# Optimization experiments

Measured on AMD Instinct MI355X. Metric: run time of the kernel, lower is better.

The kernel has to match this reference:

```python
import jax, jax.numpy as jnp
import numpy as np

N = 100000      # patches per bag
L, H, D = 1024, 512, 256   # size_dict['small']
K = 64          # k_sample
NC = 2          # n_classes


def setup_inputs() -> dict:
    key = jax.random.key(0)
    ks = jax.random.split(key, 12)
    s = 0.02
    return {
        "h": jax.random.normal(ks[0], (N, L), dtype=jnp.float32),
        "W1": jax.random.normal(ks[1], (L, H), dtype=jnp.float32) * s,
        "b1": jnp.zeros((H,), jnp.float32),
        "Wa": jax.random.normal(ks[2], (H, D), dtype=jnp.float32) * s,
        "ba": jnp.zeros((D,), jnp.float32),
        "Wb": jax.random.normal(ks[3], (H, D), dtype=jnp.float32) * s,
        "bb": jnp.zeros((D,), jnp.float32),
        "Wc": jax.random.normal(ks[4], (D, 1), dtype=jnp.float32) * s,
        "bc": jnp.zeros((1,), jnp.float32),
        "Winst": jax.random.normal(ks[5], (H, 2), dtype=jnp.float32) * s,
        "binst": jnp.zeros((2,), jnp.float32),
        "Wcls": jax.random.normal(ks[6], (H, NC), dtype=jnp.float32) * s,
        "bcls": jnp.zeros((NC,), jnp.float32),
        "label": 1,
    }


def reference(h, W1, b1, Wa, ba, Wb, bb, Wc, bc, Winst, binst, Wcls, bcls, label):
    # fc: Linear(1024,512) + ReLU
    h1 = jax.nn.relu(h @ W1 + b1)                      # [N, 512]
    # gated attention net
    a = jnp.tanh(h1 @ Wa + ba)                         # [N, 256]
    g = jax.nn.sigmoid(h1 @ Wb + bb)                   # [N, 256]
    A = (a * g) @ Wc + bc                              # [N, 1]
    A = A.T                                            # [1, N]
    A_raw = A
    A = jax.nn.softmax(A, axis=1)                      # [1, N]

    # instance evaluation: top-k / bottom-k select + gather + tiny classifier
    Asq = A[0]                                         # [N]
    _, top_p_ids = jax.lax.top_k(Asq, K)
    _, top_n_ids = jax.lax.top_k(-Asq, K)
    all_inst = jnp.concatenate([h1[top_p_ids], h1[top_n_ids]], axis=0)  # [2K, 512]
    inst_logits = all_inst @ Winst + binst             # [2K, 2]
    all_preds = jnp.argmax(inst_logits, axis=1)
    p_targets = jnp.full((K,), label, dtype=jnp.int32)
    n_targets = jnp.zeros((K,), dtype=jnp.int32)
    all_targets = jnp.concatenate([p_targets, n_targets], axis=0)
    logp = jax.nn.log_softmax(inst_logits, axis=1)
    instance_loss = -jnp.mean(logp[jnp.arange(2 * K), all_targets])

    # bag-level aggregation and classifier
    M = A @ h1                                         # [1, 512]
    logits = M @ Wcls + bcls                           # [1, n_classes]
    Y_hat = jnp.argmax(logits, axis=1, keepdims=True)
    Y_prob = jax.nn.softmax(logits, axis=1)
    return logits, Y_prob, Y_hat, A_raw, instance_loss, all_preds, all_targets
```

## Files before the change

kernel.cpp:

```cpp
#include <hip/hip_runtime.h>

#define NN 100000
#define LL 1024
#define HH 512
#define DD 256
#define TOPK 64
#define CAP 3072
#define CPB 4

#define WS_W1T   0u
#define WS_B2    1048576u
#define WS_Z     1572864u
#define Z_MNUM   0u
#define Z_SEXP   2048u
#define Z_LOSS   2052u
#define Z_CNTT   2056u
#define Z_CNTB   2060u
#define Z_HIST   2064u
#define Z_WSA    10256u
#define Z_ZWORDS 102596
#define Z_PARAMS 410384u
#define Z_SEL    410392u
#define Z_CANDT  410944u
#define Z_CANDB  423232u
#define Z_AEXT   435520u
#define Z_AEXB   447808u

typedef float  f32x16 __attribute__((ext_vector_type(16)));
typedef short  bf16x8 __attribute__((ext_vector_type(8)));

#define MFMA(a,b,c) __builtin_amdgcn_mfma_f32_32x32x16_bf16(a,b,c,0,0,0)

__device__ __forceinline__ unsigned short f2bf(float x){
  unsigned u = __float_as_uint(x);
  u += 0x7FFFu + ((u >> 16) & 1u);
  return (unsigned short)(u >> 16);
}
__device__ __forceinline__ float bf2f(unsigned short v){
  return __uint_as_float(((unsigned)v) << 16);
}
__device__ __forceinline__ unsigned sortable_u(float f){
  unsigned u = __float_as_uint(f);
  return (u & 0x80000000u) ? ~u : (u | 0x80000000u);
}

__global__ void k0_prep(const float* __restrict__ W1, const float* __restrict__ Wa,
                        const float* __restrict__ Wb,
                        unsigned short* __restrict__ W1T, unsigned short* __restrict__ B2,
                        unsigned* __restrict__ zwords)
{
  const int n1 = HH * LL;
  const int n2 = HH * HH;
  const int tot = n1 + n2 + Z_ZWORDS;
  int stride = gridDim.x * 256;
  for (int idx = blockIdx.x * 256 + threadIdx.x; idx < tot; idx += stride){
    if (idx < n1){
      int n = idx >> 10, k = idx & 1023;
      W1T[idx] = f2bf(W1[k * HH + n]);
    } else if (idx < n1 + n2){
      int j = idx - n1;
      int n = j >> 9, k = j & 511;
      int w = n >> 6, ii = n & 63;
      float v = (ii < 32) ? Wa[k * DD + (w * 32 + ii)] : Wb[k * DD + (w * 32 + ii - 32)];
      B2[j] = f2bf(v);
    } else {
      zwords[idx - n1 - n2] = 0u;
    }
  }
}

__global__ __launch_bounds__(512, 2)
void k_mega(const float* __restrict__ h, const unsigned short* __restrict__ W1T,
            const unsigned short* __restrict__ B2g,
            const float* __restrict__ b1, const float* __restrict__ ba,
            const float* __restrict__ bbg, const float* __restrict__ Wc,
            const float* __restrict__ bc,
            float* __restrict__ outA,
            float* __restrict__ wsA,
            float* __restrict__ Mnum, float* __restrict__ sum_exp)
{
  __shared__ __align__(16) unsigned short SM[64 * 512];

  const int tid  = threadIdx.x;
  const int wid  = tid >> 6;
  const int lane = tid & 63;
  const int l31  = lane & 31;
  const int half = lane >> 5;
  const int r0   = blockIdx.x * 64;

  const int sr = tid >> 3;
  const int sc = (tid & 7) << 2;
  int gr = r0 + sr; if (gr > NN - 1) gr = NN - 1;
  const float* hp = h + (size_t)gr * LL + sc;

  const unsigned short* bp0 = W1T + (size_t)(wid * 64 + l31) * LL + half * 8;
  const unsigned short* bp1 = W1T + (size_t)(wid * 64 + 32 + l31) * LL + half * 8;

  f32x16 acc00 = (f32x16)0.f, acc01 = (f32x16)0.f, acc10 = (f32x16)0.f, acc11 = (f32x16)0.f;

  float4 av = *(const float4*)hp;
  #pragma unroll 1
  for (int kc = 0; kc < 32; ++kc){
    bf16x8 b00 = *(const bf16x8*)(bp0 + kc * 32);
    bf16x8 b01 = *(const bf16x8*)(bp0 + kc * 32 + 16);
    bf16x8 b10 = *(const bf16x8*)(bp1 + kc * 32);
    bf16x8 b11 = *(const bf16x8*)(bp1 + kc * 32 + 16);

    float4 cur = av;
    if (kc < 31) av = *(const float4*)(hp + (kc + 1) * 32);
    uint2 pk;
    pk.x = (unsigned)f2bf(cur.x) | ((unsigned)f2bf(cur.y) << 16);
    pk.y = (unsigned)f2bf(cur.z) | ((unsigned)f2bf(cur.w) << 16);
    __syncthreads();
    *(uint2*)(SM + sr * 40 + sc) = pk;
    __syncthreads();

    const unsigned short* a0p = SM + l31 * 40 + half * 8;
    const unsigned short* a1p = SM + (32 + l31) * 40 + half * 8;
    bf16x8 a0k0 = *(const bf16x8*)(a0p);
    bf16x8 a1k0 = *(const bf16x8*)(a1p);
    bf16x8 a0k1 = *(const bf16x8*)(a0p + 16);
    bf16x8 a1k1 = *(const bf16x8*)(a1p + 16);
    acc00 = MFMA(a0k0, b00, acc00); acc01 = MFMA(a0k0, b10, acc01);
    acc10 = MFMA(a1k0, b00, acc10); acc11 = MFMA(a1k0, b10, acc11);
    acc00 = MFMA(a0k1, b01, acc00); acc01 = MFMA(a0k1, b11, acc01);
    acc10 = MFMA(a1k1, b01, acc10); acc11 = MFMA(a1k1, b11, acc11);
  }
  __syncthreads();

  {
    float b1v0 = b1[wid * 64 + l31];
    float b1v1 = b1[wid * 64 + 32 + l31];
    int cb0 = wid * 8 + (l31 >> 3);
    int cb1 = wid * 8 + 4 + (l31 >> 3);
    int wi = l31 & 7;
    #pragma unroll
    for (int reg = 0; reg < 16; ++reg){
      int rA = (reg & 3) + ((reg >> 2) << 3) + (half << 2);
      int rB = rA + 32;
      float v;
      v = fmaxf(acc00[reg] + b1v0, 0.f); SM[rA * 512 + ((cb0 ^ (rA & 7)) << 3) + wi] = f2bf(v);
      v = fmaxf(acc01[reg] + b1v1, 0.f); SM[rA * 512 + ((cb1 ^ (rA & 7)) << 3) + wi] = f2bf(v);
      v = fmaxf(acc10[reg] + b1v0, 0.f); SM[rB * 512 + ((cb0 ^ (rB & 7)) << 3) + wi] = f2bf(v);
      v = fmaxf(acc11[reg] + b1v1, 0.f); SM[rB * 512 + ((cb1 ^ (rB & 7)) << 3) + wi] = f2bf(v);
    }
  }
  __syncthreads();

  f32x16 q00 = (f32x16)0.f, q01 = (f32x16)0.f, q10 = (f32x16)0.f, q11 = (f32x16)0.f;
  const unsigned short* c0p = B2g + (size_t)(wid * 64 + l31) * HH + half * 8;
  const unsigned short* c1p = B2g + (size_t)(wid * 64 + 32 + l31) * HH + half * 8;
  const int m0x = l31 & 7;
  #pragma unroll 1
  for (int kc = 0; kc < 16; ++kc){
    #pragma unroll
    for (int ks = 0; ks < 2; ++ks){
      int ko = kc * 32 + ks * 16;
      int sw = (((kc * 4 + ks * 2 + half) ^ m0x) << 3);
      bf16x8 a0 = *(const bf16x8*)(SM + l31 * 512 + sw);
      bf16x8 a1 = *(const bf16x8*)(SM + (32 + l31) * 512 + sw);
      bf16x8 b0 = *(const bf16x8*)(c0p + ko);
      bf16x8 b1 = *(const bf16x8*)(c1p + ko);
      q00 = MFMA(a0, b0, q00); q01 = MFMA(a0, b1, q01);
      q10 = MFMA(a1, b0, q10); q11 = MFMA(a1, b1, q11);
    }
  }

  {
    int ca = wid * 32 + l31;
    float bav = ba[ca], bbv = bbg[ca], wcv = Wc[ca];
    #pragma unroll
    for (int mt = 0; mt < 2; ++mt){
      #pragma unroll
      for (int reg = 0; reg < 16; ++reg){
        float pav = (mt ? q10[reg] : q00[reg]) + bav;
        float pbv = (mt ? q11[reg] : q01[reg]) + bbv;
        float p = tanhf(pav) * (1.f / (1.f + expf(-pbv))) * wcv;
        p += __shfl_xor(p, 1, 64);  p += __shfl_xor(p, 2, 64);
        p += __shfl_xor(p, 4, 64);  p += __shfl_xor(p, 8, 64);
        p += __shfl_xor(p, 16, 64);
        if (l31 == 0){
          int rl = mt * 32 + (reg & 3) + ((reg >> 2) << 3) + (half << 2);
          atomicAdd(&wsA[r0 + rl], p);
        }
      }
    }
  }
  __syncthreads();
  if (tid < 64){
    int g = r0 + tid;
    if (g < NN){
      float Ar = atomicAdd(&wsA[g], 0.0f) + bc[0];
      outA[g] = Ar;
    }
  }
  __syncthreads();

  float ev = 0.f;
  { int g = r0 + lane; if (g < NN) ev = expf(outA[g]); }
  float pm = 0.f;
  const int tch = tid >> 3, twi = tid & 7;
  #pragma unroll 4
  for (int r = 0; r < 64; ++r){
    float e = __shfl(ev, r, 64);
    pm += e * bf2f(SM[r * 512 + ((tch ^ (r & 7)) << 3) + twi]);
  }
  atomicAdd(&Mnum[tid], pm);
  if (wid == 0){
    float s = ev;
    s += __shfl_xor(s, 1, 64);  s += __shfl_xor(s, 2, 64);  s += __shfl_xor(s, 4, 64);
    s += __shfl_xor(s, 8, 64);  s += __shfl_xor(s, 16, 64); s += __shfl_xor(s, 32, 64);
    if (lane == 0) atomicAdd(sum_exp, s);
  }
}

__global__ void k_hist(const float* __restrict__ A, unsigned* __restrict__ hist)
{
  __shared__ unsigned lh[2048];
  for (int i = threadIdx.x; i < 2048; i += 256) lh[i] = 0u;
  __syncthreads();
  for (int i = blockIdx.x * 256 + threadIdx.x; i < NN; i += gridDim.x * 256)
    atomicAdd(&lh[sortable_u(A[i]) >> 21], 1u);
  __syncthreads();
  for (int i = threadIdx.x; i < 2048; i += 256)
    if (lh[i]) atomicAdd(&hist[i], lh[i]);
}

__global__ void k_scan(const unsigned* __restrict__ hist, unsigned* __restrict__ params)
{
  if (threadIdx.x == 0){
    unsigned c = 0; int b = 2047;
    while (b >= 0){ c += hist[b]; if (c >= TOPK) break; --b; }
    if (b < 0) b = 0;
    int be = (b > 0) ? b - 1 : 0;
    params[0] = ((unsigned)be) << 21;
    c = 0; int b2 = 0;
    while (b2 < 2048){ c += hist[b2]; if (c >= TOPK) break; ++b2; }
    if (b2 > 2047) b2 = 2047;
    unsigned be2 = (unsigned)((b2 < 2047) ? b2 + 1 : 2047);
    params[1] = ((be2 + 1u) << 21) - 1u;
  }
}

__global__ void k_collect(const float* __restrict__ A, const unsigned* __restrict__ params,
                          unsigned* cntT, unsigned* cntB,
                          unsigned* __restrict__ candT, unsigned* __restrict__ candB)
{
  unsigned p0 = params[0], p1 = params[1];
  for (int i = blockIdx.x * 256 + threadIdx.x; i < NN; i += gridDim.x * 256){
    unsigned u = sortable_u(A[i]);
    if (u >= p0){ unsigned pos = atomicAdd(cntT, 1u); if (pos < CAP) candT[pos] = (unsigned)i; }
    if (u <= p1){ unsigned pos = atomicAdd(cntB, 1u); if (pos < CAP) candB[pos] = (unsigned)i; }
  }
}

__global__ __launch_bounds__(256)
void k_exact(const float* __restrict__ h, const float* __restrict__ W1, const float* __restrict__ b1,
             const float* __restrict__ Wa, const float* __restrict__ ba,
             const float* __restrict__ Wb, const float* __restrict__ bbg,
             const float* __restrict__ Wc, const float* __restrict__ bc,
             const unsigned* cntT, const unsigned* cntB,
             const unsigned* __restrict__ candT, const unsigned* __restrict__ candB,
             float* __restrict__ AexT, float* __restrict__ AexB)
{
  const int PB = CAP / CPB;
  int b = blockIdx.x;
  int side = (b >= PB) ? 1 : 0;
  int base = (side ? b - PB : b) * CPB;
  unsigned cnt = side ? *cntB : *cntT;
  if (cnt > CAP) cnt = CAP;
  if (base >= (int)cnt) return;
  int nc = min(CPB, (int)cnt - base);
  const unsigned* cand = side ? candB : candT;
  float* Aex = side ? AexB : AexT;

  __shared__ float hrow[CPB][LL];
  __shared__ float h1row[CPB][HH];
  __shared__ unsigned rows_s[CPB];
  __shared__ float red[4][CPB];
  int tid = threadIdx.x;
  if (tid < CPB) rows_s[tid] = cand[base + min(tid, nc - 1)];
  __syncthreads();
  for (int c = 0; c < CPB; ++c)
    ((float4*)hrow[c])[tid] = ((const float4*)(h + (size_t)rows_s[c] * LL))[tid];
  __syncthreads();

  float s0[CPB], s1[CPB];
  { float v0 = b1[tid], v1 = b1[tid + 256];
    #pragma unroll
    for (int c = 0; c < CPB; ++c){ s0[c] = v0; s1[c] = v1; } }
  for (int k = 0; k < LL; ++k){
    float w0 = W1[k * HH + tid];
    float w1 = W1[k * HH + tid + 256];
    #pragma unroll
    for (int c = 0; c < CPB; ++c){ float hv = hrow[c][k]; s0[c] += hv * w0; s1[c] += hv * w1; }
  }
  #pragma unroll
  for (int c = 0; c < CPB; ++c){
    h1row[c][tid] = fmaxf(s0[c], 0.f);
    h1row[c][tid + 256] = fmaxf(s1[c], 0.f);
  }
  __syncthreads();

  float pa[CPB], pb[CPB];
  float bav = ba[tid], bbv = bbg[tid], wcv = Wc[tid];
  #pragma unroll
  for (int c = 0; c < CPB; ++c){ pa[c] = bav; pb[c] = bbv; }
  for (int k = 0; k < HH; ++k){
    float wav = Wa[k * DD + tid];
    float wbv = Wb[k * DD + tid];
    #pragma unroll
    for (int c = 0; c < CPB; ++c){ float hv = h1row[c][k]; pa[c] += hv * wav; pb[c] += hv * wbv; }
  }
  int lane = tid & 63, w = tid >> 6;
  #pragma unroll
  for (int c = 0; c < CPB; ++c){
    float p = tanhf(pa[c]) * (1.f / (1.f + expf(-pb[c]))) * wcv;
    p += __shfl_xor(p, 1, 64);  p += __shfl_xor(p, 2, 64);  p += __shfl_xor(p, 4, 64);
    p += __shfl_xor(p, 8, 64);  p += __shfl_xor(p, 16, 64); p += __shfl_xor(p, 32, 64);
    if (lane == 0) red[w][c] = p;
  }
  __syncthreads();
  if (tid == 0)
    for (int c = 0; c < nc; ++c)
      Aex[base + c] = red[0][c] + red[1][c] + red[2][c] + red[3][c] + bc[0];
}

__global__ __launch_bounds__(256)
void k_select(const unsigned* cntT, const unsigned* cntB,
              const unsigned* __restrict__ candT, const unsigned* __restrict__ candB,
              const float* __restrict__ AexT, const float* __restrict__ AexB,
              unsigned* __restrict__ sel)
{
  __shared__ unsigned long long keys[CAP];
  __shared__ unsigned long long wmax[4];
  __shared__ unsigned long long best_s;
  int tid = threadIdx.x;
  for (int side = 0; side < 2; ++side){
    unsigned cnt = side ? *cntB : *cntT; if (cnt > CAP) cnt = CAP;
    const unsigned* cand = side ? candB : candT;
    const float* Aex = side ? AexB : AexT;
    for (int j = tid; j < (int)cnt; j += 256){
      unsigned su = sortable_u(Aex[j]);
      if (side) su = ~su;
      keys[j] = (((unsigned long long)su) << 32) | (unsigned long long)(0xFFFFFFFFu - cand[j]);
    }
    __syncthreads();
    for (int it = 0; it < TOPK; ++it){
      unsigned long long loc = 0ull;
      for (int j = tid; j < (int)cnt; j += 256){ unsigned long long k = keys[j]; loc = (k > loc) ? k : loc; }
      for (int off = 1; off < 64; off <<= 1){
        unsigned long long o = __shfl_xor(loc, off, 64);
        loc = (o > loc) ? o : loc;
      }
      if ((tid & 63) == 0) wmax[tid >> 6] = loc;
      __syncthreads();
      if (tid == 0){
        unsigned long long m01 = (wmax[0] > wmax[1]) ? wmax[0] : wmax[1];
        unsigned long long m23 = (wmax[2] > wmax[3]) ? wmax[2] : wmax[3];
        unsigned long long bb_ = (m01 > m23) ? m01 : m23;
        best_s = bb_;
        sel[side * TOPK + it] = 0xFFFFFFFFu - (unsigned)(bb_ & 0xFFFFFFFFull);
      }
      __syncthreads();
      unsigned long long bv = best_s;
      for (int j = tid; j < (int)cnt; j += 256) if (keys[j] == bv) keys[j] = 0ull;
      __syncthreads();
    }
    __syncthreads();
  }
}

__global__ __launch_bounds__(256)
void k_inst(const float* __restrict__ h, const float* __restrict__ W1, const float* __restrict__ b1,
            const float* __restrict__ Winst, const float* __restrict__ binst,
            const unsigned* __restrict__ sel, const int* __restrict__ labelp,
            float* __restrict__ out, float* __restrict__ loss_sum)
{
  __shared__ float hrow[LL];
  __shared__ float h1row[HH];
  __shared__ float red[4][2];
  int i = blockIdx.x, tid = threadIdx.x;
  unsigned row = sel[i];
  ((float4*)hrow)[tid] = ((const float4*)(h + (size_t)row * LL))[tid];
  __syncthreads();
  float s0 = b1[tid], s1 = b1[tid + 256];
  for (int k = 0; k < LL; ++k){
    float hv = hrow[k];
    s0 += hv * W1[k * HH + tid];
    s1 += hv * W1[k * HH + tid + 256];
  }
  h1row[tid] = fmaxf(s0, 0.f); h1row[tid + 256] = fmaxf(s1, 0.f);
  __syncthreads();
  float l0 = 0.f, l1 = 0.f;
  for (int d = tid; d < HH; d += 256){
    float hv = h1row[d];
    l0 += hv * Winst[d * 2];
    l1 += hv * Winst[d * 2 + 1];
  }
  for (int off = 1; off < 64; off <<= 1){ l0 += __shfl_xor(l0, off, 64); l1 += __shfl_xor(l1, off, 64); }
  if ((tid & 63) == 0){ red[tid >> 6][0] = l0; red[tid >> 6][1] = l1; }
  __syncthreads();
  if (tid == 0){
    float L0 = red[0][0] + red[1][0] + red[2][0] + red[3][0] + binst[0];
    float L1 = red[0][1] + red[1][1] + red[2][1] + red[3][1] + binst[1];
    int lab = labelp[0];
    int tgt = (i < TOPK) ? lab : 0;
    out[100006 + i] = (L1 > L0) ? 1.f : 0.f;
    out[100134 + i] = (float)tgt;
    float m = fmaxf(L0, L1);
    float lse = m + logf(expf(L0 - m) + expf(L1 - m));
    float lp = ((tgt == 1) ? L1 : L0) - lse;
    atomicAdd(loss_sum, -lp);
  }
}

__global__ __launch_bounds__(512)
void k_final(const float* __restrict__ Mnum, const float* __restrict__ sum_exp,
             const float* __restrict__ Wcls, const float* __restrict__ bcls,
             const float* __restrict__ loss_sum, float* __restrict__ out)
{
  __shared__ float red[8][2];
  int tid = threadIdx.x;
  float S = *sum_exp;
  float m = Mnum[tid] / S;
  float p0 = m * Wcls[tid * 2], p1 = m * Wcls[tid * 2 + 1];
  for (int off = 1; off < 64; off <<= 1){ p0 += __shfl_xor(p0, off, 64); p1 += __shfl_xor(p1, off, 64); }
  if ((tid & 63) == 0){ red[tid >> 6][0] = p0; red[tid >> 6][1] = p1; }
  __syncthreads();
  if (tid == 0){
    float L0 = bcls[0], L1 = bcls[1];
    for (int w = 0; w < 8; ++w){ L0 += red[w][0]; L1 += red[w][1]; }
    out[0] = L0; out[1] = L1;
    float mm = fmaxf(L0, L1);
    float e0 = expf(L0 - mm), e1 = expf(L1 - mm);
    out[2] = e0 / (e0 + e1); out[3] = e1 / (e0 + e1);
    out[4] = (L1 > L0) ? 1.f : 0.f;
    out[100005] = loss_sum[0] / 128.f;
  }
}

extern "C" void kernel_launch(void* const* d_in, const int* in_sizes, int n_in,
                              void* d_out, int out_size, void* d_ws, size_t ws_size,
                              hipStream_t stream)
{
  const float* h     = (const float*)d_in[0];
  const float* W1    = (const float*)d_in[1];
  const float* b1    = (const float*)d_in[2];
  const float* Wa    = (const float*)d_in[3];
  const float* ba    = (const float*)d_in[4];
  const float* Wb    = (const float*)d_in[5];
  const float* bbg   = (const float*)d_in[6];
  const float* Wc    = (const float*)d_in[7];
  const float* bc    = (const float*)d_in[8];
  const float* Winst = (const float*)d_in[9];
  const float* binst = (const float*)d_in[10];
  const float* Wcls  = (const float*)d_in[11];
  const float* bcls  = (const float*)d_in[12];
  const int*   label = (const int*)d_in[13];
  float* out = (float*)d_out;

  char* ws = (char*)d_ws;
  unsigned short* W1T = (unsigned short*)(ws + WS_W1T);
  unsigned short* B2  = (unsigned short*)(ws + WS_B2);
  char* Z = ws + WS_Z;
  float*    Mnum   = (float*)(Z + Z_MNUM);
  float*    sexp   = (float*)(Z + Z_SEXP);
  float*    lsum   = (float*)(Z + Z_LOSS);
  unsigned* cntT   = (unsigned*)(Z + Z_CNTT);
  unsigned* cntB   = (unsigned*)(Z + Z_CNTB);
  unsigned* hist   = (unsigned*)(Z + Z_HIST);
  float*    wsA    = (float*)(Z + Z_WSA);
  unsigned* params = (unsigned*)(Z + Z_PARAMS);
  unsigned* sel    = (unsigned*)(Z + Z_SEL);
  unsigned* candT  = (unsigned*)(Z + Z_CANDT);
  unsigned* candB  = (unsigned*)(Z + Z_CANDB);
  float*    AexT   = (float*)(Z + Z_AEXT);
  float*    AexB   = (float*)(Z + Z_AEXB);

  k0_prep<<<1024, 256, 0, stream>>>(W1, Wa, Wb, W1T, B2, (unsigned*)Z);
  k_mega<<<1563, 512, 0, stream>>>(h, W1T, B2, b1, ba, bbg, Wc, bc,
                                   out + 5, wsA, Mnum, sexp);
  k_hist<<<400, 256, 0, stream>>>(out + 5, hist);
  k_scan<<<1, 64, 0, stream>>>(hist, params);
  k_collect<<<400, 256, 0, stream>>>(out + 5, params, cntT, cntB, candT, candB);
  k_exact<<<2 * (CAP / CPB), 256, 0, stream>>>(h, W1, b1, Wa, ba, Wb, bbg, Wc, bc,
                                               cntT, cntB, candT, candB, AexT, AexB);
  k_select<<<1, 256, 0, stream>>>(cntT, cntB, candT, candB, AexT, AexB, sel);
  k_inst<<<128, 256, 0, stream>>>(h, W1, b1, Winst, binst, sel, label, out, lsum);
  k_final<<<1, 512, 0, stream>>>(Mnum, sexp, Wcls, bcls, lsum, out);
}
```

Measured before the change: 1.226 ms.

## Double-buffer GEMM A-tile, coalesce weight prep, refine top-k threshold with second histogram

```diff
diff --git a/kernel.cpp b/kernel.cpp
--- a/kernel.cpp
+++ b/kernel.cpp
@@ -7,6 +7,7 @@
 #define TOPK 64
 #define CAP 3072
 #define CPB 4
+#define DELTA 3e-3f
 
 #define WS_W1T   0u
 #define WS_B2    1048576u
@@ -18,13 +19,13 @@
 #define Z_CNTB   2060u
 #define Z_HIST   2064u
 #define Z_WSA    10256u
-#define Z_ZWORDS 102596
 #define Z_PARAMS 410384u
-#define Z_SEL    410392u
-#define Z_CANDT  410944u
-#define Z_CANDB  423232u
-#define Z_AEXT   435520u
-#define Z_AEXB   447808u
+#define Z_SEL    410416u
+#define Z_CANDT  410928u
+#define Z_CANDB  423216u
+#define Z_AEXT   435504u
+#define Z_AEXB   447792u
+#define Z_ZWORDS 108876
 
 typedef float  f32x16 __attribute__((ext_vector_type(16)));
 typedef short  bf16x8 __attribute__((ext_vector_type(8)));
@@ -42,6 +43,15 @@
 __device__ __forceinline__ unsigned sortable_u(float f){
   unsigned u = __float_as_uint(f);
   return (u & 0x80000000u) ? ~u : (u | 0x80000000u);
+}
+__device__ __forceinline__ float inv_sortable(unsigned u){
+  unsigned orig = (u & 0x80000000u) ? (u ^ 0x80000000u) : ~u;
+  return __uint_as_float(orig);
+}
+__device__ __forceinline__ unsigned cvtpk(float lo, float hi){
+  unsigned r;
+  asm("v_cvt_pk_bf16_f32 %0, %1, %2" : "=v"(r) : "v"(lo), "v"(hi));
+  return r;
 }
 
 __global__ void k0_prep(const float* __restrict__ W1, const float* __restrict__ Wa,
@@ -55,14 +65,14 @@
   int stride = gridDim.x * 256;
   for (int idx = blockIdx.x * 256 + threadIdx.x; idx < tot; idx += stride){
     if (idx < n1){
-      int n = idx >> 10, k = idx & 1023;
-      W1T[idx] = f2bf(W1[k * HH + n]);
+      int k = idx >> 9, n = idx & 511;
+      W1T[(size_t)n * LL + k] = f2bf(W1[idx]);
     } else if (idx < n1 + n2){
       int j = idx - n1;
-      int n = j >> 9, k = j & 511;
+      int k = j >> 9, n = j & 511;
       int w = n >> 6, ii = n & 63;
       float v = (ii < 32) ? Wa[k * DD + (w * 32 + ii)] : Wb[k * DD + (w * 32 + ii - 32)];
-      B2[j] = f2bf(v);
+      B2[(size_t)n * HH + k] = f2bf(v);
     } else {
       zwords[idx - n1 - n2] = 0u;
     }
@@ -98,33 +108,50 @@
 
   f32x16 acc00 = (f32x16)0.f, acc01 = (f32x16)0.f, acc10 = (f32x16)0.f, acc11 = (f32x16)0.f;
 
-  float4 av = *(const float4*)hp;
+  unsigned short* sbuf0 = SM;
+  unsigned short* sbuf1 = SM + 2560;
+
+  float4 av;
+  {
+    float4 a0 = *(const float4*)(hp);
+    av = *(const float4*)(hp + 32);
+    uint2 pk; pk.x = cvtpk(a0.x, a0.y); pk.y = cvtpk(a0.z, a0.w);
+    *(uint2*)(sbuf0 + sr * 40 + sc) = pk;
+  }
+  asm volatile("s_waitcnt lgkmcnt(0)" ::: "memory");
+  __builtin_amdgcn_s_barrier();
+  __builtin_amdgcn_sched_barrier(0);
+
+  unsigned short* rb = sbuf0;
+  unsigned short* wb = sbuf1;
+
   #pragma unroll 1
   for (int kc = 0; kc < 32; ++kc){
     bf16x8 b00 = *(const bf16x8*)(bp0 + kc * 32);
+    bf16x8 b10 = *(const bf16x8*)(bp1 + kc * 32);
     bf16x8 b01 = *(const bf16x8*)(bp0 + kc * 32 + 16);
-    bf16x8 b10 = *(const bf16x8*)(bp1 + kc * 32);
     bf16x8 b11 = *(const bf16x8*)(bp1 + kc * 32 + 16);
-
+    __builtin_amdgcn_sched_barrier(0);
     float4 cur = av;
-    if (kc < 31) av = *(const float4*)(hp + (kc + 1) * 32);
-    uint2 pk;
-    pk.x = (unsigned)f2bf(cur.x) | ((unsigned)f2bf(cur.y) << 16);
-    pk.y = (unsigned)f2bf(cur.z) | ((unsigned)f2bf(cur.w) << 16);
-    __syncthreads();
-    *(uint2*)(SM + sr * 40 + sc) = pk;
-    __syncthreads();
-
-    const unsigned short* a0p = SM + l31 * 40 + half * 8;
-    const unsigned short* a1p = SM + (32 + l31) * 40 + half * 8;
+    av = *(const float4*)(hp + min(kc + 2, 31) * 32);
+    __builtin_amdgcn_sched_barrier(0);
+    uint2 pk; pk.x = cvtpk(cur.x, cur.y); pk.y = cvtpk(cur.z, cur.w);
+    *(uint2*)(wb + sr * 40 + sc) = pk;
+    const unsigned short* a0p = rb + l31 * 40 + half * 8;
+    const unsigned short* a1p = rb + (32 + l31) * 40 + half * 8;
     bf16x8 a0k0 = *(const bf16x8*)(a0p);
     bf16x8 a1k0 = *(const bf16x8*)(a1p);
+    acc00 = MFMA(a0k0, b00, acc00); acc01 = MFMA(a0k0, b10, acc01);
+    acc10 = MFMA(a1k0, b00, acc10); acc11 = MFMA(a1k0, b10, acc11);
     bf16x8 a0k1 = *(const bf16x8*)(a0p + 16);
     bf16x8 a1k1 = *(const bf16x8*)(a1p + 16);
-    acc00 = MFMA(a0k0, b00, acc00); acc01 = MFMA(a0k0, b10, acc01);
-    acc10 = MFMA(a1k0, b00, acc10); acc11 = MFMA(a1k0, b10, acc11);
     acc00 = MFMA(a0k1, b01, acc00); acc01 = MFMA(a0k1, b11, acc01);
     acc10 = MFMA(a1k1, b01, acc10); acc11 = MFMA(a1k1, b11, acc11);
+    { unsigned short* t = rb; rb = wb; wb = t; }
+    asm volatile("s_waitcnt lgkmcnt(0)" ::: "memory");
+    __builtin_amdgcn_sched_barrier(0);
+    __builtin_amdgcn_s_barrier();
+    __builtin_amdgcn_sched_barrier(0);
   }
   __syncthreads();
 
@@ -229,16 +256,71 @@
 __global__ void k_scan(const unsigned* __restrict__ hist, unsigned* __restrict__ params)
 {
   if (threadIdx.x == 0){
-    unsigned c = 0; int b = 2047;
-    while (b >= 0){ c += hist[b]; if (c >= TOPK) break; --b; }
+    unsigned c = 0, hh = 0; int b = 2047;
+    for (; b >= 0; --b){ hh = hist[b]; c += hh; if (c >= TOPK) break; }
     if (b < 0) b = 0;
-    int be = (b > 0) ? b - 1 : 0;
-    params[0] = ((unsigned)be) << 21;
-    c = 0; int b2 = 0;
-    while (b2 < 2048){ c += hist[b2]; if (c >= TOPK) break; ++b2; }
+    params[2] = (unsigned)b;
+    params[4] = TOPK - (c - hh);
+    c = 0; hh = 0; int b2 = 0;
+    for (; b2 < 2048; ++b2){ hh = hist[b2]; c += hh; if (c >= TOPK) break; }
     if (b2 > 2047) b2 = 2047;
-    unsigned be2 = (unsigned)((b2 < 2047) ? b2 + 1 : 2047);
-    params[1] = ((be2 + 1u) << 21) - 1u;
+    params[3] = (unsigned)b2;
+    params[5] = TOPK - (c - hh);
+  }
+}
+
+__global__ void k_hist2(const float* __restrict__ A, const unsigned* __restrict__ params,
+                        unsigned* __restrict__ h2T, unsigned* __restrict__ h2B)
+{
+  __shared__ unsigned lh[4096];
+  for (int i = threadIdx.x; i < 4096; i += 256) lh[i] = 0u;
+  __syncthreads();
+  unsigned bT = params[2], bB = params[3];
+  for (int i = blockIdx.x * 256 + threadIdx.x; i < NN; i += gridDim.x * 256){
+    unsigned u = sortable_u(A[i]);
+    unsigned b = u >> 21;
+    if (b == bT) atomicAdd(&lh[(u >> 10) & 2047u], 1u);
+    if (b == bB) atomicAdd(&lh[2048 + ((u >> 10) & 2047u)], 1u);
+  }
+  __syncthreads();
+  for (int i = threadIdx.x; i < 2048; i += 256){
+    if (lh[i])        atomicAdd(&h2T[i], lh[i]);
+    if (lh[2048 + i]) atomicAdd(&h2B[i], lh[2048 + i]);
+  }
+}
+
+__global__ __launch_bounds__(128)
+void k_scan2(const unsigned* __restrict__ h2T, const unsigned* __restrict__ h2B,
+             unsigned* __restrict__ params)
+{
+  int side = threadIdx.x >> 6;
+  int lane = threadIdx.x & 63;
+  const unsigned* h2 = side ? h2B : h2T;
+  unsigned bT  = params[2 + side];
+  unsigned rem = params[4 + side];
+  unsigned cs = 0;
+  int base = lane * 32;
+  #pragma unroll 4
+  for (int j = 0; j < 32; ++j) cs += h2[base + j];
+  unsigned before = 0;
+  for (int j = 0; j < 64; ++j){
+    unsigned v = __shfl(cs, j, 64);
+    bool earlier = side ? (j < lane) : (j > lane);
+    if (earlier) before += v;
+  }
+  if (before < rem && before + cs >= rem){
+    unsigned c = before; int s = base;
+    if (side == 0){
+      for (int b = base + 31; b >= base; --b){ c += h2[b]; if (c >= rem){ s = b; break; } }
+      unsigned ulo = (bT << 21) | ((unsigned)s << 10);
+      float v = inv_sortable(ulo) - DELTA;
+      params[0] = sortable_u(v);
+    } else {
+      for (int b = base; b < base + 32; ++b){ c += h2[b]; if (c >= rem){ s = b; break; } }
+      unsigned uhi = (bT << 21) | ((unsigned)s << 10) | 1023u;
+      float v = inv_sortable(uhi) + DELTA;
+      params[1] = sortable_u(v);
+    }
   }
 }
 
@@ -477,12 +559,16 @@
   unsigned* candB  = (unsigned*)(Z + Z_CANDB);
   float*    AexT   = (float*)(Z + Z_AEXT);
   float*    AexB   = (float*)(Z + Z_AEXB);
+  unsigned* h2T    = (unsigned*)(Z + Z_CANDT);
+  unsigned* h2B    = (unsigned*)(Z + Z_CANDB);
 
   k0_prep<<<1024, 256, 0, stream>>>(W1, Wa, Wb, W1T, B2, (unsigned*)Z);
   k_mega<<<1563, 512, 0, stream>>>(h, W1T, B2, b1, ba, bbg, Wc, bc,
                                    out + 5, wsA, Mnum, sexp);
   k_hist<<<400, 256, 0, stream>>>(out + 5, hist);
   k_scan<<<1, 64, 0, stream>>>(hist, params);
+  k_hist2<<<400, 256, 0, stream>>>(out + 5, params, h2T, h2B);
+  k_scan2<<<1, 128, 0, stream>>>(h2T, h2B, params);
   k_collect<<<400, 256, 0, stream>>>(out + 5, params, cntT, cntB, candT, candB);
   k_exact<<<2 * (CAP / CPB), 256, 0, stream>>>(h, W1, b1, Wa, ba, Wb, bbg, Wc, bc,
                                                cntT, cntB, candT, candB, AexT, AexB);
```

Measured after the change: 1.165 ms. 1.05x faster.
